# Optimization experiments

Hardware: AMD Instinct MI355X
Metric: run time of the kernel (lower is better)

The kernel has to match this reference:

```python
import jax, jax.numpy as jnp
import numpy as np

SEQ_LEN = 4096
INPUT_DIM = 768
DIM = 512
NUM_HEADS = 8
HEAD_DIM = DIM // NUM_HEADS
WINDOW_SIZE = 7
DILATION = 8
HALF_WINDOW = WINDOW_SIZE // 2  # 3
BIDIRECTIONAL = True


def _dilated_mask(seq_len):
    # allowed neighbors of query i: j = i + k*DILATION for k in [-HALF_WINDOW, HALF_WINDOW]
    # (only k<=0 if not bidirectional), clipped to [0, seq_len)
    idx = jnp.arange(seq_len)
    d = idx[None, :] - idx[:, None]  # j - i
    allowed = (d % DILATION == 0) & (jnp.abs(d) <= DILATION * HALF_WINDOW)
    if not BIDIRECTIONAL:
        allowed = allowed & (d <= 0)
    return jnp.where(allowed, 0.0, -jnp.inf).astype(jnp.float32)  # [S, S]


def setup_inputs() -> dict:
    key = jax.random.key(0)
    ks = jax.random.split(key, 6)
    s = 0.02
    return {
        "x": jax.random.normal(ks[0], (SEQ_LEN, INPUT_DIM), dtype=jnp.float32),
        "W_in": jax.random.normal(ks[1], (INPUT_DIM, DIM), dtype=jnp.float32) * s,
        "b_in": jnp.zeros((DIM,), dtype=jnp.float32),
        "W_tse": jax.random.normal(ks[2], (DIM, 3 * DIM), dtype=jnp.float32) * s,
        "W_out": jax.random.normal(ks[3], (DIM, DIM), dtype=jnp.float32) * s,
        "b_out": jnp.zeros((DIM,), dtype=jnp.float32),
    }


def reference(x, W_in, b_in, W_tse, W_out, b_out):
    S = x.shape[0]
    scale = HEAD_DIM ** -0.5
    h = x @ W_in + b_in                                   # [S, DIM]
    tse = (h @ W_tse).reshape(S, 3, NUM_HEADS, HEAD_DIM)   # [S, 3, H, hd]
    q, k, v = tse[:, 0], tse[:, 1], tse[:, 2]              # each [S, H, hd]
    scores = jnp.einsum("shd,thd->hst", q, k) * scale      # [H, S, S]
    scores = scores + _dilated_mask(S)[None, :, :]
    attn = jax.nn.softmax(scores, axis=-1)                 # [H, S, S]
    out = jnp.einsum("hst,thd->shd", attn, v)              # [S, H, hd]
    out = out.reshape(S, DIM)
    return out @ W_out + b_out                              # [S, DIM]
```

## Files before the change

### kernel.cpp

```cpp
#include <hip/hip_runtime.h>
#include <hip/hip_bf16.h>

#define S_LEN 4096
#define IN_DIM 768
#define D_DIM 512
#define N_HEADS 8
#define H_DIM 64
#define TSE_DIM 1536

typedef __attribute__((ext_vector_type(8))) short frag8;
typedef __attribute__((ext_vector_type(4))) float f32x4;

__device__ __forceinline__ unsigned short f2bfbits(float f) {
    unsigned int u = __float_as_uint(f);
    unsigned int r = (u + 0x7FFFu + ((u >> 16) & 1u)) >> 16;
    return (unsigned short)r;
}
__device__ __forceinline__ float bf2f(unsigned short b) {
    return __uint_as_float(((unsigned int)b) << 16);
}

__device__ __forceinline__ void gload_lds16(const void* g, void* l) {
    __builtin_amdgcn_global_load_lds(
        (const __attribute__((address_space(1))) unsigned int*)g,
        (__attribute__((address_space(3))) unsigned int*)l,
        16, 0, 0);
}

__global__ __launch_bounds__(256) void prep_kernel(
        const float4* __restrict__ x4, ushort4* __restrict__ xb4,
        const float* __restrict__ W_in,  unsigned short* __restrict__ WinT,
        const float* __restrict__ W_tse, unsigned short* __restrict__ WtseT,
        const float* __restrict__ W_out, unsigned short* __restrict__ WoutT) {
    __shared__ float tile[32][33];
    int b = blockIdx.x;
    if (b < 3072) {
        int i = b * 256 + threadIdx.x;
        float4 v = x4[i];
        ushort4 o;
        o.x = f2bfbits(v.x); o.y = f2bfbits(v.y);
        o.z = f2bfbits(v.z); o.w = f2bfbits(v.w);
        xb4[i] = o;
        return;
    }
    const float* in; unsigned short* out; int K, N, t;
    if (b < 3456)      { t = b - 3072; in = W_in;  out = WinT;  K = IN_DIM; N = D_DIM;  }
    else if (b < 4224) { t = b - 3456; in = W_tse; out = WtseT; K = D_DIM;  N = TSE_DIM;}
    else               { t = b - 4224; in = W_out; out = WoutT; K = D_DIM;  N = D_DIM;  }
    int ktiles = K / 32;
    int kb = (t % ktiles) * 32, nb = (t / ktiles) * 32;
    int tx = threadIdx.x & 31, ty = threadIdx.x >> 5;
    #pragma unroll
    for (int r = ty; r < 32; r += 8)
        tile[r][tx] = in[(size_t)(kb + r) * N + nb + tx];
    __syncthreads();
    #pragma unroll
    for (int r = ty; r < 32; r += 8)
        out[(size_t)(nb + r) * K + kb + tx] = f2bfbits(tile[tx][r]);
}

template<bool OUT_BF16, bool BIAS>
__global__ __launch_bounds__(256) void gemm_nt(
        const unsigned short* __restrict__ A,
        const unsigned short* __restrict__ Bt,
        const float* __restrict__ bias,
        void* __restrict__ C,
        int M, int N, int K) {
    __shared__ __align__(16) unsigned short As[3][64 * 32];
    __shared__ __align__(16) unsigned short Bs[3][64 * 32];

    const int bm = blockIdx.x * 64;
    const int bn = blockIdx.y * 64;
    const int lane = threadIdx.x & 63;
    const int wave = threadIdx.x >> 6;
    const int wr = wave >> 1;
    const int wc = wave & 1;
    const int fr = lane & 15;
    const int fg = lane >> 4;

    const int srow = lane >> 2;
    const int scol = (lane & 3) * 8;

    const unsigned short* agp = A  + (size_t)(bm + wave * 16 + srow) * K + scol;
    const unsigned short* bgp = Bt + (size_t)(bn + wave * 16 + srow) * K + scol;
    unsigned short* const alp = &As[0][wave * 512];
    unsigned short* const blp = &Bs[0][wave * 512];

    f32x4 acc[2][2];
    #pragma unroll
    for (int mi = 0; mi < 2; ++mi)
        #pragma unroll
        for (int ni = 0; ni < 2; ++ni)
            acc[mi][ni] = (f32x4)(0.f);

    const int nt = K >> 5;

    gload_lds16(agp, alp);
    gload_lds16(bgp, blp);
    gload_lds16(agp + 32, alp + 2048);
    gload_lds16(bgp + 32, blp + 2048);

    for (int kt = 0; kt < nt; ++kt) {
        if (kt == nt - 1) asm volatile("s_waitcnt vmcnt(0)" ::: "memory");
        else              asm volatile("s_waitcnt vmcnt(2)" ::: "memory");
        __builtin_amdgcn_s_barrier();
        __builtin_amdgcn_sched_barrier(0);

        if (kt + 2 < nt) {
            const int sb = (kt + 2) % 3;
            gload_lds16(agp + (size_t)(kt + 2) * 32, alp + sb * 2048);
            gload_lds16(bgp + (size_t)(kt + 2) * 32, blp + sb * 2048);
        }

        const int cb = kt % 3;
        frag8 a[2], b[2];
        #pragma unroll
        for (int mi = 0; mi < 2; ++mi)
            a[mi] = *(const frag8*)&As[cb][(wr * 32 + mi * 16 + fr) * 32 + fg * 8];
        #pragma unroll
        for (int ni = 0; ni < 2; ++ni)
            b[ni] = *(const frag8*)&Bs[cb][(wc * 32 + ni * 16 + fr) * 32 + fg * 8];
        #pragma unroll
        for (int mi = 0; mi < 2; ++mi)
            #pragma unroll
            for (int ni = 0; ni < 2; ++ni)
                acc[mi][ni] = __builtin_amdgcn_mfma_f32_16x16x32_bf16(
                        a[mi], b[ni], acc[mi][ni], 0, 0, 0);
    }

    #pragma unroll
    for (int mi = 0; mi < 2; ++mi) {
        int grow = bm + wr * 32 + mi * 16 + fg * 4;
        #pragma unroll
        for (int ni = 0; ni < 2; ++ni) {
            int gcol = bn + wc * 32 + ni * 16 + fr;
            float bv = BIAS ? bias[gcol] : 0.f;
            #pragma unroll
            for (int r = 0; r < 4; ++r) {
                float v = acc[mi][ni][r] + bv;
                if (OUT_BF16)
                    ((unsigned short*)C)[(size_t)(grow + r) * N + gcol] = f2bfbits(v);
                else
                    ((float*)C)[(size_t)(grow + r) * N + gcol] = v;
            }
        }
    }
}

__global__ __launch_bounds__(256) void attn_kernel(
        const unsigned short* __restrict__ tse, unsigned short* __restrict__ out) {
    const int s    = blockIdx.x * 4 + (threadIdx.x >> 6);
    const int lane = threadIdx.x & 63;
    const int off  = (lane >> 3) * H_DIM + (lane & 7) * 8;

    float qf[8];
    {
        frag8 q = *(const frag8*)(tse + (size_t)s * TSE_DIM + off);
        #pragma unroll
        for (int i = 0; i < 8; ++i) qf[i] = bf2f((unsigned short)q[i]);
    }

    float sc[7];
    #pragma unroll
    for (int j = 0; j < 7; ++j) {
        int t = s + (j - 3) * 8;
        bool valid = (t >= 0) && (t < S_LEN);
        float p = 0.f;
        if (valid) {
            frag8 k = *(const frag8*)(tse + (size_t)t * TSE_DIM + D_DIM + off);
            #pragma unroll
            for (int i = 0; i < 8; ++i) p += qf[i] * bf2f((unsigned short)k[i]);
        }
        p += __shfl_xor(p, 1, 64);
        p += __shfl_xor(p, 2, 64);
        p += __shfl_xor(p, 4, 64);
        sc[j] = valid ? p * 0.125f : -__builtin_inff();
    }

    float m = sc[0];
    #pragma unroll
    for (int j = 1; j < 7; ++j) m = fmaxf(m, sc[j]);

    float w[7], denom = 0.f;
    #pragma unroll
    for (int j = 0; j < 7; ++j) {
        w[j] = (sc[j] == -__builtin_inff()) ? 0.f : __expf(sc[j] - m);
        denom += w[j];
    }
    const float inv = 1.f / denom;

    float of[8];
    #pragma unroll
    for (int i = 0; i < 8; ++i) of[i] = 0.f;
    #pragma unroll
    for (int j = 0; j < 7; ++j) {
        int t = s + (j - 3) * 8;
        if (t >= 0 && t < S_LEN) {
            frag8 v = *(const frag8*)(tse + (size_t)t * TSE_DIM + 2 * D_DIM + off);
            #pragma unroll
            for (int i = 0; i < 8; ++i) of[i] += w[j] * bf2f((unsigned short)v[i]);
        }
    }

    frag8 o;
    #pragma unroll
    for (int i = 0; i < 8; ++i) o[i] = (short)f2bfbits(of[i] * inv);
    *(frag8*)(out + (size_t)s * D_DIM + off) = o;
}

extern "C" void kernel_launch(void* const* d_in, const int* in_sizes, int n_in,
                              void* d_out, int out_size, void* d_ws, size_t ws_size,
                              hipStream_t stream) {
    (void)in_sizes; (void)n_in; (void)out_size;
    const float* x     = (const float*)d_in[0];
    const float* W_in  = (const float*)d_in[1];
    const float* b_in  = (const float*)d_in[2];
    const float* W_tse = (const float*)d_in[3];
    const float* W_out = (const float*)d_in[4];
    const float* b_out = (const float*)d_in[5];

    char* p = (char*)d_ws;
    unsigned short* xb    = (unsigned short*)p; p += (size_t)S_LEN * IN_DIM * 2;
    unsigned short* WinT  = (unsigned short*)p; p += (size_t)D_DIM * IN_DIM * 2;
    unsigned short* WtseT = (unsigned short*)p; p += (size_t)TSE_DIM * D_DIM * 2;
    unsigned short* WoutT = (unsigned short*)p; p += (size_t)D_DIM * D_DIM * 2;
    unsigned short* h     = (unsigned short*)p; p += (size_t)S_LEN * D_DIM * 2;
    unsigned short* tse   = (unsigned short*)p; p += (size_t)S_LEN * TSE_DIM * 2;
    unsigned short* attn  = (unsigned short*)p; p += (size_t)S_LEN * D_DIM * 2;
    if ((size_t)(p - (char*)d_ws) > ws_size) return;

    prep_kernel<<<4480, 256, 0, stream>>>(
            (const float4*)x, (ushort4*)xb, W_in, WinT, W_tse, WtseT, W_out, WoutT);

    gemm_nt<true, true><<<dim3(S_LEN / 64, D_DIM / 64), 256, 0, stream>>>(
            xb, WinT, b_in, h, S_LEN, D_DIM, IN_DIM);
    gemm_nt<true, false><<<dim3(S_LEN / 64, TSE_DIM / 64), 256, 0, stream>>>(
            h, WtseT, nullptr, tse, S_LEN, TSE_DIM, D_DIM);
    attn_kernel<<<S_LEN / 4, 256, 0, stream>>>(tse, attn);
    gemm_nt<false, true><<<dim3(S_LEN / 64, D_DIM / 64), 256, 0, stream>>>(
            attn, WoutT, b_out, (float*)d_out, S_LEN, D_DIM, D_DIM);
}
```

Baseline: 56.01 us.

## Replace 4-wave GEMM with single-wave 32x64 tile GEMM and compile-time K

The shared-memory GEMM used for the three projections changes from a 256-thread block with a 64x64 tile split over four waves to a 64-thread, single-wave block computing a 32x64 tile with 2x4 MFMA accumulators. K becomes a template parameter so the k-loop fully unrolls, and the per-iteration s_barrier goes away because one wave does its own loads and waits on vmcnt counts. The goal is to drop block-level synchronisation and raise the number of independent blocks. The cost is less A/B reuse per block, more blocks, and more global traffic per FLOP.

```diff
diff --git a/kernel.cpp b/kernel.cpp
--- a/kernel.cpp
+++ b/kernel.cpp
@@ -59,81 +59,79 @@
         out[(size_t)(nb + r) * K + kb + tx] = f2bfbits(tile[tx][r]);
 }
 
-template<bool OUT_BF16, bool BIAS>
-__global__ __launch_bounds__(256) void gemm_nt(
+template<int K, bool OUT_BF16, bool BIAS>
+__global__ __launch_bounds__(64) void gemm1w(
         const unsigned short* __restrict__ A,
         const unsigned short* __restrict__ Bt,
         const float* __restrict__ bias,
         void* __restrict__ C,
-        int M, int N, int K) {
-    __shared__ __align__(16) unsigned short As[3][64 * 32];
+        int M, int N) {
+    constexpr int NT = K >> 5;
+    __shared__ __align__(16) unsigned short As[3][32 * 32];
     __shared__ __align__(16) unsigned short Bs[3][64 * 32];
 
-    const int bm = blockIdx.x * 64;
+    const int bm = blockIdx.x * 32;
     const int bn = blockIdx.y * 64;
-    const int lane = threadIdx.x & 63;
-    const int wave = threadIdx.x >> 6;
-    const int wr = wave >> 1;
-    const int wc = wave & 1;
+    const int lane = threadIdx.x;
     const int fr = lane & 15;
     const int fg = lane >> 4;
-
     const int srow = lane >> 2;
     const int scol = (lane & 3) * 8;
 
-    const unsigned short* agp = A  + (size_t)(bm + wave * 16 + srow) * K + scol;
-    const unsigned short* bgp = Bt + (size_t)(bn + wave * 16 + srow) * K + scol;
-    unsigned short* const alp = &As[0][wave * 512];
-    unsigned short* const blp = &Bs[0][wave * 512];
-
-    f32x4 acc[2][2];
+    const unsigned short* ag = A  + (size_t)(bm + srow) * K + scol;
+    const unsigned short* bg = Bt + (size_t)(bn + srow) * K + scol;
+
+    f32x4 acc[2][4];
     #pragma unroll
     for (int mi = 0; mi < 2; ++mi)
         #pragma unroll
-        for (int ni = 0; ni < 2; ++ni)
+        for (int ni = 0; ni < 4; ++ni)
             acc[mi][ni] = (f32x4)(0.f);
 
-    const int nt = K >> 5;
-
-    gload_lds16(agp, alp);
-    gload_lds16(bgp, blp);
-    gload_lds16(agp + 32, alp + 2048);
-    gload_lds16(bgp + 32, blp + 2048);
-
-    for (int kt = 0; kt < nt; ++kt) {
-        if (kt == nt - 1) asm volatile("s_waitcnt vmcnt(0)" ::: "memory");
-        else              asm volatile("s_waitcnt vmcnt(2)" ::: "memory");
-        __builtin_amdgcn_s_barrier();
-        __builtin_amdgcn_sched_barrier(0);
-
-        if (kt + 2 < nt) {
-            const int sb = (kt + 2) % 3;
-            gload_lds16(agp + (size_t)(kt + 2) * 32, alp + sb * 2048);
-            gload_lds16(bgp + (size_t)(kt + 2) * 32, blp + sb * 2048);
-        }
+    #define STAGE(t, bf)                                                        \
+        {                                                                       \
+            _Pragma("unroll")                                                   \
+            for (int i = 0; i < 2; ++i)                                         \
+                gload_lds16(ag + (size_t)i * 16 * K + (t) * 32, &As[bf][i * 512]); \
+            _Pragma("unroll")                                                   \
+            for (int i = 0; i < 4; ++i)                                         \
+                gload_lds16(bg + (size_t)i * 16 * K + (t) * 32, &Bs[bf][i * 512]); \
+        }
+
+    STAGE(0, 0)
+    STAGE(1, 1)
+
+    #pragma unroll
+    for (int kt = 0; kt < NT; ++kt) {
+        if (kt + 2 < NT) STAGE(kt + 2, (kt + 2) % 3)
+
+        if (kt + 2 < NT)      asm volatile("s_waitcnt vmcnt(12)" ::: "memory");
+        else if (kt + 1 < NT) asm volatile("s_waitcnt vmcnt(6)"  ::: "memory");
+        else                  asm volatile("s_waitcnt vmcnt(0)"  ::: "memory");
 
         const int cb = kt % 3;
-        frag8 a[2], b[2];
+        frag8 a[2], b[4];
         #pragma unroll
         for (int mi = 0; mi < 2; ++mi)
-            a[mi] = *(const frag8*)&As[cb][(wr * 32 + mi * 16 + fr) * 32 + fg * 8];
-        #pragma unroll
-        for (int ni = 0; ni < 2; ++ni)
-            b[ni] = *(const frag8*)&Bs[cb][(wc * 32 + ni * 16 + fr) * 32 + fg * 8];
+            a[mi] = *(const frag8*)&As[cb][(mi * 16 + fr) * 32 + fg * 8];
+        #pragma unroll
+        for (int ni = 0; ni < 4; ++ni)
+            b[ni] = *(const frag8*)&Bs[cb][(ni * 16 + fr) * 32 + fg * 8];
         #pragma unroll
         for (int mi = 0; mi < 2; ++mi)
             #pragma unroll
-            for (int ni = 0; ni < 2; ++ni)
+            for (int ni = 0; ni < 4; ++ni)
                 acc[mi][ni] = __builtin_amdgcn_mfma_f32_16x16x32_bf16(
                         a[mi], b[ni], acc[mi][ni], 0, 0, 0);
     }
+    #undef STAGE
 
     #pragma unroll
     for (int mi = 0; mi < 2; ++mi) {
-        int grow = bm + wr * 32 + mi * 16 + fg * 4;
-        #pragma unroll
-        for (int ni = 0; ni < 2; ++ni) {
-            int gcol = bn + wc * 32 + ni * 16 + fr;
+        int grow = bm + mi * 16 + fg * 4;
+        #pragma unroll
+        for (int ni = 0; ni < 4; ++ni) {
+            int gcol = bn + ni * 16 + fr;
             float bv = BIAS ? bias[gcol] : 0.f;
             #pragma unroll
             for (int r = 0; r < 4; ++r) {
@@ -232,11 +230,11 @@
     prep_kernel<<<4480, 256, 0, stream>>>(
             (const float4*)x, (ushort4*)xb, W_in, WinT, W_tse, WtseT, W_out, WoutT);
 
-    gemm_nt<true, true><<<dim3(S_LEN / 64, D_DIM / 64), 256, 0, stream>>>(
-            xb, WinT, b_in, h, S_LEN, D_DIM, IN_DIM);
-    gemm_nt<true, false><<<dim3(S_LEN / 64, TSE_DIM / 64), 256, 0, stream>>>(
-            h, WtseT, nullptr, tse, S_LEN, TSE_DIM, D_DIM);
+    gemm1w<IN_DIM, true, true><<<dim3(S_LEN / 32, D_DIM / 64), 64, 0, stream>>>(
+            xb, WinT, b_in, h, S_LEN, D_DIM);
+    gemm1w<D_DIM, true, false><<<dim3(S_LEN / 32, TSE_DIM / 64), 64, 0, stream>>>(
+            h, WtseT, nullptr, tse, S_LEN, TSE_DIM);
     attn_kernel<<<S_LEN / 4, 256, 0, stream>>>(tse, attn);
-    gemm_nt<false, true><<<dim3(S_LEN / 64, D_DIM / 64), 256, 0, stream>>>(
-            attn, WoutT, b_out, (float*)d_out, S_LEN, D_DIM, D_DIM);
-}
+    gemm1w<D_DIM, false, true><<<dim3(S_LEN / 32, D_DIM / 64), 64, 0, stream>>>(
+            attn, WoutT, b_out, (float*)d_out, S_LEN, D_DIM);
+}
```

New measurement: 59.35 us. 6.0% more time.
